# Kernel optimization log

Measured on AMD Instinct MI355X. Metric: run time of the kernel, lower is better.

Reference implementation:

```python
import jax, jax.numpy as jnp
import numpy as np

B, V, S, E, K, FF = 16, 512, 1024, 8, 2, 2048  # batch, n_vars, seq_len, n_experts, top_k, ff_dim


def setup_inputs() -> dict:
    key = jax.random.key(0)
    ks = jax.random.split(key, 6)
    def w(k, shape, fan_in):
        return (jax.random.normal(k, shape, jnp.float32) / np.sqrt(fan_in)).astype(jnp.float32)
    return {
        "x": jax.random.normal(ks[0], (B, S, V), jnp.float32),
        "gate_W": w(ks[1], (E, S), S),          # Gating: Linear(seq_len -> n_experts), no bias
        "exp_W": w(ks[2], (E, S, S), S),        # per-expert Linear(seq_len -> seq_len) weights
        "exp_b": jnp.zeros((E, S), jnp.float32),
        "fc1_W": w(ks[3], (FF, V), V),          # MLPFeat fc1: Linear(n_vars -> ff_dim)
        "fc1_b": jnp.zeros((FF,), jnp.float32),
        "fc2_W": w(ks[4], (V, FF), FF),         # MLPFeat fc2: Linear(ff_dim -> n_vars)
        "fc2_b": jnp.zeros((V,), jnp.float32),
    }


def reference(x, gate_W, exp_W, exp_b, fc1_W, fc1_b, fc2_W, fc2_b):
    # Dropout layers are identity at inference.
    res = x                                   # [B,S,V]
    xt = jnp.swapaxes(x, 1, 2)                # [B,V,S] tokens of dim seq_len

    # --- MLPTime (multi_expert MoE) ---
    logits = jnp.einsum('bvs,es->bve', xt, gate_W)      # [B,V,E]
    probs = jax.nn.softmax(logits, axis=-1)             # gate_logits returned by torch code
    w, sel = jax.lax.top_k(probs, K)                    # [B,V,K]
    # combine top-k weights into a dense per-expert weight [B,V,E] (zeros off top-k)
    full_w = jnp.sum(jax.nn.one_hot(sel, E, dtype=xt.dtype) * w[..., None], axis=2)
    # all-expert outputs, then weighted combine (same math as the per-expert scatter loop)
    all_out = jnp.einsum('bvs,eos->bveo', xt, exp_W) + exp_b[None, None]  # [B,V,E,S]
    moe = jnp.einsum('bve,bveo->bvo', full_w, all_out)                    # [B,V,S]
    t = jax.nn.relu(moe)

    x = jnp.swapaxes(t, 1, 2) + res           # [B,S,V] residual

    # --- MLPFeat ---
    res2 = x
    h = jax.nn.relu(x @ fc1_W.T + fc1_b)      # [B,S,FF]
    x = h @ fc2_W.T + fc2_b + res2            # [B,S,V]
    return (x, probs)
```

## Files before the change

### kernel.cpp

```cpp
#include <hip/hip_runtime.h>
#include <stdint.h>

#define B_  16
#define V_  512
#define S_  1024
#define E_  8
#define FF_ 2048
#define NT_ (B_*V_)
#define NR_ (B_*S_)

typedef __attribute__((ext_vector_type(8))) short bf16x8;
typedef __attribute__((ext_vector_type(4))) float f32x4;

__device__ __forceinline__ unsigned short f2bf(float f) {
    unsigned int u = __float_as_uint(f);
    u += 0x7FFFu + ((u >> 16) & 1u);
    return (unsigned short)(u >> 16);
}
__device__ __forceinline__ float bf2f(unsigned short u) {
    return __uint_as_float(((unsigned int)u) << 16);
}

__device__ __forceinline__ void gl_lds16(const void* g, void* l) {
    __builtin_amdgcn_global_load_lds((const __attribute__((address_space(1))) void*)g,
                                     (__attribute__((address_space(3))) void*)l,
                                     16, 0, 0);
}

__device__ __forceinline__ void cvt4(const float* s, unsigned short* d, int i) {
    float4 v = *(const float4*)(s + i);
    ushort4 o; o.x = f2bf(v.x); o.y = f2bf(v.y); o.z = f2bf(v.z); o.w = f2bf(v.w);
    *(ushort4*)(d + i) = o;
}
__global__ void k_convert3(const float* __restrict__ s0, unsigned short* __restrict__ d0, int g0,
                           const float* __restrict__ s1, unsigned short* __restrict__ d1, int g1,
                           const float* __restrict__ s2, unsigned short* __restrict__ d2) {
    int g = blockIdx.x * 256 + threadIdx.x;
    if (g < g0)           cvt4(s0, d0, g * 4);
    else if (g < g0 + g1) cvt4(s1, d1, (g - g0) * 4);
    else                  cvt4(s2, d2, (g - g0 - g1) * 4);
}

__global__ void k_transpose_xt(const float* __restrict__ x, unsigned short* __restrict__ xt) {
    __shared__ float t[32][33];
    int b = blockIdx.z, st = blockIdx.y, vt = blockIdx.x;
    int col = threadIdx.x & 31, row8 = threadIdx.x >> 5;
    for (int r = 0; r < 4; ++r) {
        int sl = row8 + r * 8;
        t[sl][col] = x[(b * S_ + st * 32 + sl) * V_ + vt * 32 + col];
    }
    __syncthreads();
    for (int r = 0; r < 4; ++r) {
        int vl = row8 + r * 8;
        xt[(size_t)(b * V_ + vt * 32 + vl) * S_ + st * 32 + col] = f2bf(t[col][vl]);
    }
}

__global__ __launch_bounds__(256) void k_gate_part(const float* __restrict__ x,
                                                   const float* __restrict__ gate_W,
                                                   double* __restrict__ part,
                                                   int* __restrict__ cnt) {
    __shared__ float gw[E_ * 128];
    __shared__ double red[4 * 64 * E_];
    int sc = blockIdx.x, vt0 = blockIdx.y * 64, b = blockIdx.z;
    int tid = threadIdx.x;
    if (sc == 0 && blockIdx.y == 0 && b == 0 && tid < E_) cnt[tid] = 0;
    for (int i = tid; i < E_ * 128; i += 256) {
        int e = i >> 7, j = i & 127;
        gw[i] = gate_W[e * S_ + sc * 128 + j];
    }
    __syncthreads();
    int vl = tid & 63, sg = tid >> 6;
    double acc[E_];
    #pragma unroll
    for (int e = 0; e < E_; ++e) acc[e] = 0.0;
    for (int jj = sg; jj < 128; jj += 4) {
        int s = sc * 128 + jj;
        double xv = (double)x[(b * S_ + s) * V_ + vt0 + vl];
        #pragma unroll
        for (int e = 0; e < E_; ++e) acc[e] += xv * (double)gw[e * 128 + jj];
    }
    #pragma unroll
    for (int e = 0; e < E_; ++e) red[(sg * 64 + vl) * E_ + e] = acc[e];
    __syncthreads();
    for (int i = tid; i < 64 * E_; i += 256) {
        int tkn = i >> 3, e = i & 7;
        double s = red[(0 * 64 + tkn) * E_ + e] + red[(1 * 64 + tkn) * E_ + e]
                 + red[(2 * 64 + tkn) * E_ + e] + red[(3 * 64 + tkn) * E_ + e];
        int t = b * V_ + vt0 + tkn;
        part[((size_t)sc * NT_ + t) * E_ + e] = s;
    }
}

__global__ __launch_bounds__(256) void k_gate_fin(const double* __restrict__ part,
                                                  float* __restrict__ probs_out,
                                                  int* __restrict__ cnt, int* __restrict__ tok_of,
                                                  int* __restrict__ tk_slot, float* __restrict__ tk_w) {
    int t = blockIdx.x * 256 + threadIdx.x;
    int lane = threadIdx.x & 63;
    double l[E_];
    #pragma unroll
    for (int e = 0; e < E_; ++e) l[e] = 0.0;
    for (int c = 0; c < S_ / 128; ++c) {
        const double* p = part + ((size_t)c * NT_ + t) * E_;
        #pragma unroll
        for (int e = 0; e < E_; ++e) l[e] += p[e];
    }
    double m = l[0];
    #pragma unroll
    for (int e = 1; e < E_; ++e) m = l[e] > m ? l[e] : m;
    double p[E_], sum = 0.0;
    #pragma unroll
    for (int e = 0; e < E_; ++e) { p[e] = exp(l[e] - m); sum += p[e]; }
    float pf[E_];
    #pragma unroll
    for (int e = 0; e < E_; ++e) pf[e] = (float)(p[e] / sum);
    float4 pa = {pf[0], pf[1], pf[2], pf[3]}, pb = {pf[4], pf[5], pf[6], pf[7]};
    *(float4*)(probs_out + (size_t)t * E_) = pa;
    *(float4*)(probs_out + (size_t)t * E_ + 4) = pb;
    int i0 = 0;
    #pragma unroll
    for (int e = 1; e < E_; ++e) if (pf[e] > pf[i0]) i0 = e;
    int i1 = -1;
    #pragma unroll
    for (int e = 0; e < E_; ++e) if (e != i0 && (i1 < 0 || pf[e] > pf[i1])) i1 = e;
    int sel[2] = {i0, i1};
    float wsel[2] = {pf[i0], pf[i1]};
    #pragma unroll
    for (int k = 0; k < 2; ++k) {
        int ie = sel[k];
        int pos = 0;
        for (int e = 0; e < E_; ++e) {
            unsigned long long msk = __ballot(ie == e);
            if (ie == e) {
                int rank = __popcll(msk & ((1ull << lane) - 1ull));
                int leader = __ffsll((long long)msk) - 1;
                int base = 0;
                if (lane == leader) base = atomicAdd(&cnt[e], __popcll(msk));
                base = __shfl(base, leader);
                pos = base + rank;
            }
        }
        tok_of[ie * NT_ + pos] = t;
        tk_slot[t * 2 + k] = (ie << 16) | pos;
        tk_w[t * 2 + k] = wsel[k];
    }
}

__global__ void k_scan(const int* __restrict__ cnt, int* __restrict__ offs,
                       int* __restrict__ tile_hdr) {
    if (threadIdx.x == 0) {
        int o = 0, nt = 0;
        for (int e = 0; e < E_; ++e) {
            offs[e] = o;
            for (int p = 0; p < cnt[e]; p += 128) {
                tile_hdr[1 + nt * 2] = e;
                tile_hdr[2 + nt * 2] = p;
                ++nt;
            }
            o += cnt[e];
        }
        offs[E_] = o;
        tile_hdr[0] = nt;
    }
}

__device__ __forceinline__ void gemm_k_loop64(const unsigned short* (&ap)[4],
                                              const unsigned short* (&bp)[4],
                                              short* As, short* Bs, int kIters, int wave, int lane,
                                              f32x4 (&acc)[4][4]) {
    char* ldsA = (char*)As + wave * 4096;
    char* ldsB = (char*)Bs + wave * 4096;
    int wm = (wave & 1) << 6, wn = (wave >> 1) << 6;
    int lr = lane & 15, quad = lane >> 4;
    int pb = (quad ^ (lr & 7)) * 8;
    const unsigned short* a0 = ap[0]; const unsigned short* a1 = ap[1];
    const unsigned short* a2 = ap[2]; const unsigned short* a3 = ap[3];
    const unsigned short* b0 = bp[0]; const unsigned short* b1 = bp[1];
    const unsigned short* b2 = bp[2]; const unsigned short* b3 = bp[3];
    for (int kk = 0; kk < kIters; ++kk) {
        gl_lds16(a0, ldsA);        gl_lds16(a1, ldsA + 1024);
        gl_lds16(a2, ldsA + 2048); gl_lds16(a3, ldsA + 3072);
        gl_lds16(b0, ldsB);        gl_lds16(b1, ldsB + 1024);
        gl_lds16(b2, ldsB + 2048); gl_lds16(b3, ldsB + 3072);
        a0 += 64; a1 += 64; a2 += 64; a3 += 64;
        b0 += 64; b1 += 64; b2 += 64; b3 += 64;
        __syncthreads();
        #pragma unroll
        for (int ks = 0; ks < 2; ++ks) {
            int po = pb ^ (ks << 5);
            bf16x8 af[4], bfv[4];
            #pragma unroll
            for (int i = 0; i < 4; ++i)
                af[i] = *(const bf16x8*)(As + (wm + i * 16 + lr) * 64 + po);
            #pragma unroll
            for (int j = 0; j < 4; ++j)
                bfv[j] = *(const bf16x8*)(Bs + (wn + j * 16 + lr) * 64 + po);
            #pragma unroll
            for (int i = 0; i < 4; ++i)
                #pragma unroll
                for (int j = 0; j < 4; ++j)
                    acc[i][j] = __builtin_amdgcn_mfma_f32_16x16x32_bf16(af[i], bfv[j], acc[i][j], 0, 0, 0);
        }
        __syncthreads();
    }
}

__global__ __launch_bounds__(256, 3) void k_moe_gemm(const unsigned short* __restrict__ xt,
                                                     const unsigned short* __restrict__ expWb,
                                                     const float* __restrict__ exp_b,
                                                     const int* __restrict__ cnt, const int* __restrict__ offs,
                                                     const int* __restrict__ tok_of,
                                                     const int* __restrict__ tile_hdr,
                                                     unsigned short* __restrict__ Yb) {
    int ntl = tile_hdr[0];
    if ((int)blockIdx.x >= ntl) return;
    int e    = tile_hdr[1 + blockIdx.x * 2];
    int pos0 = tile_hdr[2 + blockIdx.x * 2];
    int ne = cnt[e];
    int nt = blockIdx.y;
    __shared__ __align__(16) short As[128 * 64];
    __shared__ __align__(16) short Bs[128 * 64];
    int tid = threadIdx.x, wave = tid >> 6, lane = tid & 63;
    int rowLoc = wave * 32 + (lane >> 3);
    int cg = ((lane & 7) ^ ((lane >> 3) & 7)) * 8;
    const unsigned short* Wb = expWb + (size_t)e * S_ * S_;
    const unsigned short* ap[4];
    const unsigned short* bp[4];
    #pragma unroll
    for (int c = 0; c < 4; ++c) {
        int rr = rowLoc + c * 8;
        int tok = tok_of[e * NT_ + min(pos0 + rr, ne - 1)];
        ap[c] = xt + (size_t)tok * S_ + cg;
        bp[c] = Wb + (size_t)(nt * 128 + rr) * S_ + cg;
    }
    f32x4 acc[4][4] = {};
    gemm_k_loop64(ap, bp, As, Bs, S_ / 64, wave, lane, acc);
    int wm = (wave & 1) << 6, wn = (wave >> 1) << 6;
    int lr = lane & 15, quad = lane >> 4;
    int yrow0 = offs[e];
    #pragma unroll
    for (int i = 0; i < 4; ++i)
        #pragma unroll
        for (int r = 0; r < 4; ++r) {
            int pos = pos0 + wm + i * 16 + quad * 4 + r;
            if (pos < ne) {
                size_t row = (size_t)(yrow0 + pos);
                #pragma unroll
                for (int j = 0; j < 4; ++j) {
                    int col = nt * 128 + wn + j * 16 + lr;
                    Yb[row * S_ + col] = f2bf(acc[i][j][r] + exp_b[e * S_ + col]);
                }
            }
        }
}

__global__ void k_combine(const float* __restrict__ x, const unsigned short* __restrict__ Yb,
                          const int* __restrict__ offs, const int* __restrict__ tk_slot,
                          const float* __restrict__ tk_w,
                          unsigned short* __restrict__ x2b) {
    __shared__ float t[32][33];
    int b = blockIdx.z, st = blockIdx.y, vt = blockIdx.x;
    int tid = threadIdx.x;
    int vl = tid >> 3, sq = (tid & 7) * 4;
    int tok = b * V_ + vt * 32 + vl;
    int s0 = tk_slot[tok * 2 + 0], s1 = tk_slot[tok * 2 + 1];
    float w0 = tk_w[tok * 2 + 0], w1 = tk_w[tok * 2 + 1];
    size_t r0 = (size_t)(offs[s0 >> 16] + (s0 & 0xFFFF));
    size_t r1 = (size_t)(offs[s1 >> 16] + (s1 & 0xFFFF));
    int sg = st * 32 + sq;
    ushort4 y0 = *(const ushort4*)(Yb + r0 * S_ + sg);
    ushort4 y1 = *(const ushort4*)(Yb + r1 * S_ + sg);
    t[vl][sq + 0] = fmaxf(w0 * bf2f(y0.x) + w1 * bf2f(y1.x), 0.f);
    t[vl][sq + 1] = fmaxf(w0 * bf2f(y0.y) + w1 * bf2f(y1.y), 0.f);
    t[vl][sq + 2] = fmaxf(w0 * bf2f(y0.z) + w1 * bf2f(y1.z), 0.f);
    t[vl][sq + 3] = fmaxf(w0 * bf2f(y0.w) + w1 * bf2f(y1.w), 0.f);
    __syncthreads();
    int vcol = tid & 31, srow8 = tid >> 5;
    for (int r = 0; r < 4; ++r) {
        int sl = srow8 + r * 8;
        size_t gi = (size_t)(b * S_ + st * 32 + sl) * V_ + vt * 32 + vcol;
        x2b[gi] = f2bf(x[gi] + t[vcol][sl]);
    }
}

__global__ __launch_bounds__(256, 3) void k_fc1(const unsigned short* __restrict__ x2b,
                                                const unsigned short* __restrict__ w1b,
                                                const float* __restrict__ fc1_b,
                                                unsigned short* __restrict__ h) {
    __shared__ __align__(16) short As[128 * 64];
    __shared__ __align__(16) short Bs[128 * 64];
    int tid = threadIdx.x, wave = tid >> 6, lane = tid & 63;
    int rowLoc = wave * 32 + (lane >> 3);
    int cg = ((lane & 7) ^ ((lane >> 3) & 7)) * 8;
    int m0 = blockIdx.x * 128, n0 = blockIdx.y * 128;
    const unsigned short* ap[4];
    const unsigned short* bp[4];
    #pragma unroll
    for (int c = 0; c < 4; ++c) {
        int rr = rowLoc + c * 8;
        ap[c] = x2b + (size_t)(m0 + rr) * V_ + cg;
        bp[c] = w1b + (size_t)(n0 + rr) * V_ + cg;
    }
    f32x4 acc[4][4] = {};
    gemm_k_loop64(ap, bp, As, Bs, V_ / 64, wave, lane, acc);
    int wm = (wave & 1) << 6, wn = (wave >> 1) << 6;
    int lr = lane & 15, quad = lane >> 4;
    #pragma unroll
    for (int i = 0; i < 4; ++i)
        #pragma unroll
        for (int r = 0; r < 4; ++r) {
            size_t row = (size_t)(m0 + wm + i * 16 + quad * 4 + r);
            #pragma unroll
            for (int j = 0; j < 4; ++j) {
                int col = n0 + wn + j * 16 + lr;
                h[row * FF_ + col] = f2bf(fmaxf(acc[i][j][r] + fc1_b[col], 0.f));
            }
        }
}

__global__ __launch_bounds__(256, 3) void k_fc2(const unsigned short* __restrict__ h,
                                                const unsigned short* __restrict__ w2b,
                                                const float* __restrict__ fc2_b,
                                                const unsigned short* __restrict__ x2b,
                                                float* __restrict__ out) {
    __shared__ __align__(16) short As[128 * 64];
    __shared__ __align__(16) short Bs[128 * 64];
    int tid = threadIdx.x, wave = tid >> 6, lane = tid & 63;
    int rowLoc = wave * 32 + (lane >> 3);
    int cg = ((lane & 7) ^ ((lane >> 3) & 7)) * 8;
    int m0 = blockIdx.x * 128, n0 = blockIdx.y * 128;
    const unsigned short* ap[4];
    const unsigned short* bp[4];
    #pragma unroll
    for (int c = 0; c < 4; ++c) {
        int rr = rowLoc + c * 8;
        ap[c] = h + (size_t)(m0 + rr) * FF_ + cg;
        bp[c] = w2b + (size_t)(n0 + rr) * FF_ + cg;
    }
    f32x4 acc[4][4] = {};
    gemm_k_loop64(ap, bp, As, Bs, FF_ / 64, wave, lane, acc);
    int wm = (wave & 1) << 6, wn = (wave >> 1) << 6;
    int lr = lane & 15, quad = lane >> 4;
    #pragma unroll
    for (int i = 0; i < 4; ++i)
        #pragma unroll
        for (int r = 0; r < 4; ++r) {
            size_t row = (size_t)(m0 + wm + i * 16 + quad * 4 + r);
            #pragma unroll
            for (int j = 0; j < 4; ++j) {
                int col = n0 + wn + j * 16 + lr;
                out[row * V_ + col] = acc[i][j][r] + fc2_b[col] + bf2f(x2b[row * V_ + col]);
            }
        }
}

extern "C" void kernel_launch(void* const* d_in, const int* in_sizes, int n_in,
                              void* d_out, int out_size, void* d_ws, size_t ws_size,
                              hipStream_t stream) {
    const float* x      = (const float*)d_in[0];
    const float* gate_W = (const float*)d_in[1];
    const float* exp_W  = (const float*)d_in[2];
    const float* exp_b  = (const float*)d_in[3];
    const float* fc1_W  = (const float*)d_in[4];
    const float* fc1_b  = (const float*)d_in[5];
    const float* fc2_W  = (const float*)d_in[6];
    const float* fc2_b  = (const float*)d_in[7];
    float* out_x = (float*)d_out;
    float* out_p = (float*)d_out + (size_t)B_ * S_ * V_;

    if (ws_size < (size_t)155582592) return;

    char* ws = (char*)d_ws;
    unsigned short* Yb    = (unsigned short*)(ws);
    unsigned short* xt    = (unsigned short*)(ws +  67108864);
    int*            tile_hdr = (int*)(ws + 83886080);
    unsigned short* x2b   = (unsigned short*)(ws + 117440512);
    unsigned short* expWb = (unsigned short*)(ws + 134217728);
    unsigned short* fc1Wb = (unsigned short*)(ws + 150994944);
    unsigned short* fc2Wb = (unsigned short*)(ws + 153092096);
    char* route = ws + 155189248;
    int*   cnt     = (int*)(route);
    int*   offs    = (int*)(route + 64);
    int*   tok_of  = (int*)(route + 128);
    int*   tk_slot = (int*)(route + 128 + 262144);
    float* tk_w    = (float*)(route + 128 + 262144 + 65536);
    unsigned short* h = (unsigned short*)ws;
    double* part = (double*)ws;

    k_convert3<<<dim3((2097152 + 262144 + 262144) / 256), 256, 0, stream>>>(
        exp_W, expWb, 2097152, fc1_W, fc1Wb, 262144, fc2_W, fc2Wb);
    k_transpose_xt<<<dim3(V_ / 32, S_ / 32, B_), 256, 0, stream>>>(x, xt);
    k_gate_part<<<dim3(S_ / 128, V_ / 64, B_), 256, 0, stream>>>(x, gate_W, part, cnt);
    k_gate_fin<<<dim3(NT_ / 256), 256, 0, stream>>>(part, out_p, cnt, tok_of, tk_slot, tk_w);
    k_scan<<<1, 64, 0, stream>>>(cnt, offs, tile_hdr);
    k_moe_gemm<<<dim3(136, S_ / 128), 256, 0, stream>>>(xt, expWb, exp_b, cnt, offs, tok_of, tile_hdr, Yb);
    k_combine<<<dim3(V_ / 32, S_ / 32, B_), 256, 0, stream>>>(x, Yb, offs, tk_slot, tk_w, x2b);
    k_fc1<<<dim3(NR_ / 128, FF_ / 128), 256, 0, stream>>>(x2b, fc1Wb, fc1_b, h);
    k_fc2<<<dim3(NR_ / 128, V_ / 128), 256, 0, stream>>>(h, fc2Wb, fc2_b, x2b, out_x);
}
```

Measured before the change: 330.5 us.

## Fuse gate logits into transpose kernel and drop the scan kernel

Gate partial logits are now computed inside the x transpose kernel, reusing the shared-memory tile, so x is read only once and the separate gate-partial launch is removed. The single-thread scan kernel is gone: the MoE GEMM derives its expert and row offset from cnt on the fly, and the combine kernel recomputes per-expert prefix offsets itself. The GEMM tile index is also remapped across blockIdx.x, which changes which expert tiles sit next to each other in launch order. In exchange, part grows to 32 partial chunks instead of 8, so gate_fin reads four times as much data, and each thread does a short serial dot product in double precision.

After: 312.7 us. 1.06x faster.

```diff
diff --git a/kernel.cpp b/kernel.cpp
--- a/kernel.cpp
+++ b/kernel.cpp
@@ -41,55 +41,33 @@
     else                  cvt4(s2, d2, (g - g0 - g1) * 4);
 }
 
-__global__ void k_transpose_xt(const float* __restrict__ x, unsigned short* __restrict__ xt) {
+__global__ __launch_bounds__(256) void k_xt_gate(const float* __restrict__ x,
+                                                 const float* __restrict__ gate_W,
+                                                 unsigned short* __restrict__ xt,
+                                                 double* __restrict__ part,
+                                                 int* __restrict__ cnt) {
     __shared__ float t[32][33];
+    __shared__ float gw[E_][32];
     int b = blockIdx.z, st = blockIdx.y, vt = blockIdx.x;
-    int col = threadIdx.x & 31, row8 = threadIdx.x >> 5;
+    int tid = threadIdx.x;
+    if (vt == 0 && st == 0 && b == 0 && tid < E_) cnt[tid] = 0;
+    int col = tid & 31, row8 = tid >> 5;
     for (int r = 0; r < 4; ++r) {
         int sl = row8 + r * 8;
         t[sl][col] = x[(b * S_ + st * 32 + sl) * V_ + vt * 32 + col];
     }
+    gw[row8][col] = gate_W[row8 * S_ + st * 32 + col];
     __syncthreads();
     for (int r = 0; r < 4; ++r) {
         int vl = row8 + r * 8;
         xt[(size_t)(b * V_ + vt * 32 + vl) * S_ + st * 32 + col] = f2bf(t[col][vl]);
     }
-}
-
-__global__ __launch_bounds__(256) void k_gate_part(const float* __restrict__ x,
-                                                   const float* __restrict__ gate_W,
-                                                   double* __restrict__ part,
-                                                   int* __restrict__ cnt) {
-    __shared__ float gw[E_ * 128];
-    __shared__ double red[4 * 64 * E_];
-    int sc = blockIdx.x, vt0 = blockIdx.y * 64, b = blockIdx.z;
-    int tid = threadIdx.x;
-    if (sc == 0 && blockIdx.y == 0 && b == 0 && tid < E_) cnt[tid] = 0;
-    for (int i = tid; i < E_ * 128; i += 256) {
-        int e = i >> 7, j = i & 127;
-        gw[i] = gate_W[e * S_ + sc * 128 + j];
-    }
-    __syncthreads();
-    int vl = tid & 63, sg = tid >> 6;
-    double acc[E_];
-    #pragma unroll
-    for (int e = 0; e < E_; ++e) acc[e] = 0.0;
-    for (int jj = sg; jj < 128; jj += 4) {
-        int s = sc * 128 + jj;
-        double xv = (double)x[(b * S_ + s) * V_ + vt0 + vl];
-        #pragma unroll
-        for (int e = 0; e < E_; ++e) acc[e] += xv * (double)gw[e * 128 + jj];
-    }
-    #pragma unroll
-    for (int e = 0; e < E_; ++e) red[(sg * 64 + vl) * E_ + e] = acc[e];
-    __syncthreads();
-    for (int i = tid; i < 64 * E_; i += 256) {
-        int tkn = i >> 3, e = i & 7;
-        double s = red[(0 * 64 + tkn) * E_ + e] + red[(1 * 64 + tkn) * E_ + e]
-                 + red[(2 * 64 + tkn) * E_ + e] + red[(3 * 64 + tkn) * E_ + e];
-        int t = b * V_ + vt0 + tkn;
-        part[((size_t)sc * NT_ + t) * E_ + e] = s;
-    }
+    double acc = 0.0;
+    #pragma unroll
+    for (int s = 0; s < 32; ++s)
+        acc += (double)t[s][col] * (double)gw[row8][s];
+    int tok = b * V_ + vt * 32 + col;
+    part[((size_t)st * NT_ + tok) * E_ + row8] = acc;
 }
 
 __global__ __launch_bounds__(256) void k_gate_fin(const double* __restrict__ part,
@@ -101,7 +79,7 @@
     double l[E_];
     #pragma unroll
     for (int e = 0; e < E_; ++e) l[e] = 0.0;
-    for (int c = 0; c < S_ / 128; ++c) {
+    for (int c = 0; c < S_ / 32; ++c) {
         const double* p = part + ((size_t)c * NT_ + t) * E_;
         #pragma unroll
         for (int e = 0; e < E_; ++e) l[e] += p[e];
@@ -144,24 +122,6 @@
         tok_of[ie * NT_ + pos] = t;
         tk_slot[t * 2 + k] = (ie << 16) | pos;
         tk_w[t * 2 + k] = wsel[k];
-    }
-}
-
-__global__ void k_scan(const int* __restrict__ cnt, int* __restrict__ offs,
-                       int* __restrict__ tile_hdr) {
-    if (threadIdx.x == 0) {
-        int o = 0, nt = 0;
-        for (int e = 0; e < E_; ++e) {
-            offs[e] = o;
-            for (int p = 0; p < cnt[e]; p += 128) {
-                tile_hdr[1 + nt * 2] = e;
-                tile_hdr[2 + nt * 2] = p;
-                ++nt;
-            }
-            o += cnt[e];
-        }
-        offs[E_] = o;
-        tile_hdr[0] = nt;
     }
 }
 
@@ -209,15 +169,22 @@
 __global__ __launch_bounds__(256, 3) void k_moe_gemm(const unsigned short* __restrict__ xt,
                                                      const unsigned short* __restrict__ expWb,
                                                      const float* __restrict__ exp_b,
-                                                     const int* __restrict__ cnt, const int* __restrict__ offs,
+                                                     const int* __restrict__ cnt,
                                                      const int* __restrict__ tok_of,
-                                                     const int* __restrict__ tile_hdr,
                                                      unsigned short* __restrict__ Yb) {
-    int ntl = tile_hdr[0];
-    if ((int)blockIdx.x >= ntl) return;
-    int e    = tile_hdr[1 + blockIdx.x * 2];
-    int pos0 = tile_hdr[2 + blockIdx.x * 2];
-    int ne = cnt[e];
+    int bx = ((int)(blockIdx.x & 7)) * 17 + (int)(blockIdx.x >> 3);
+    int e = -1, pos0 = 0, yrow0 = 0, ne = 0;
+    {
+        int tb = 0, o = 0;
+        #pragma unroll
+        for (int i = 0; i < E_; ++i) {
+            int ci = cnt[i];
+            int nti = (ci + 127) >> 7;
+            if (e < 0 && bx < tb + nti) { e = i; pos0 = (bx - tb) * 128; yrow0 = o; ne = ci; }
+            tb += nti; o += ci;
+        }
+    }
+    if (e < 0) return;
     int nt = blockIdx.y;
     __shared__ __align__(16) short As[128 * 64];
     __shared__ __align__(16) short Bs[128 * 64];
@@ -238,7 +205,6 @@
     gemm_k_loop64(ap, bp, As, Bs, S_ / 64, wave, lane, acc);
     int wm = (wave & 1) << 6, wn = (wave >> 1) << 6;
     int lr = lane & 15, quad = lane >> 4;
-    int yrow0 = offs[e];
     #pragma unroll
     for (int i = 0; i < 4; ++i)
         #pragma unroll
@@ -256,7 +222,7 @@
 }
 
 __global__ void k_combine(const float* __restrict__ x, const unsigned short* __restrict__ Yb,
-                          const int* __restrict__ offs, const int* __restrict__ tk_slot,
+                          const int* __restrict__ cnt, const int* __restrict__ tk_slot,
                           const float* __restrict__ tk_w,
                           unsigned short* __restrict__ x2b) {
     __shared__ float t[32][33];
@@ -266,8 +232,16 @@
     int tok = b * V_ + vt * 32 + vl;
     int s0 = tk_slot[tok * 2 + 0], s1 = tk_slot[tok * 2 + 1];
     float w0 = tk_w[tok * 2 + 0], w1 = tk_w[tok * 2 + 1];
-    size_t r0 = (size_t)(offs[s0 >> 16] + (s0 & 0xFFFF));
-    size_t r1 = (size_t)(offs[s1 >> 16] + (s1 & 0xFFFF));
+    int e0 = s0 >> 16, e1 = s1 >> 16;
+    int r0b = 0, r1b = 0, o = 0;
+    #pragma unroll
+    for (int i = 0; i < E_; ++i) {
+        if (i == e0) r0b = o;
+        if (i == e1) r1b = o;
+        o += cnt[i];
+    }
+    size_t r0 = (size_t)(r0b + (s0 & 0xFFFF));
+    size_t r1 = (size_t)(r1b + (s1 & 0xFFFF));
     int sg = st * 32 + sq;
     ushort4 y0 = *(const ushort4*)(Yb + r0 * S_ + sg);
     ushort4 y1 = *(const ushort4*)(Yb + r1 * S_ + sg);
@@ -374,14 +348,12 @@
     char* ws = (char*)d_ws;
     unsigned short* Yb    = (unsigned short*)(ws);
     unsigned short* xt    = (unsigned short*)(ws +  67108864);
-    int*            tile_hdr = (int*)(ws + 83886080);
     unsigned short* x2b   = (unsigned short*)(ws + 117440512);
     unsigned short* expWb = (unsigned short*)(ws + 134217728);
     unsigned short* fc1Wb = (unsigned short*)(ws + 150994944);
     unsigned short* fc2Wb = (unsigned short*)(ws + 153092096);
     char* route = ws + 155189248;
     int*   cnt     = (int*)(route);
-    int*   offs    = (int*)(route + 64);
     int*   tok_of  = (int*)(route + 128);
     int*   tk_slot = (int*)(route + 128 + 262144);
     float* tk_w    = (float*)(route + 128 + 262144 + 65536);
@@ -390,12 +362,10 @@
 
     k_convert3<<<dim3((2097152 + 262144 + 262144) / 256), 256, 0, stream>>>(
         exp_W, expWb, 2097152, fc1_W, fc1Wb, 262144, fc2_W, fc2Wb);
-    k_transpose_xt<<<dim3(V_ / 32, S_ / 32, B_), 256, 0, stream>>>(x, xt);
-    k_gate_part<<<dim3(S_ / 128, V_ / 64, B_), 256, 0, stream>>>(x, gate_W, part, cnt);
+    k_xt_gate<<<dim3(V_ / 32, S_ / 32, B_), 256, 0, stream>>>(x, gate_W, xt, part, cnt);
     k_gate_fin<<<dim3(NT_ / 256), 256, 0, stream>>>(part, out_p, cnt, tok_of, tk_slot, tk_w);
-    k_scan<<<1, 64, 0, stream>>>(cnt, offs, tile_hdr);
-    k_moe_gemm<<<dim3(136, S_ / 128), 256, 0, stream>>>(xt, expWb, exp_b, cnt, offs, tok_of, tile_hdr, Yb);
-    k_combine<<<dim3(V_ / 32, S_ / 32, B_), 256, 0, stream>>>(x, Yb, offs, tk_slot, tk_w, x2b);
+    k_moe_gemm<<<dim3(136, S_ / 128), 256, 0, stream>>>(xt, expWb, exp_b, cnt, tok_of, Yb);
+    k_combine<<<dim3(V_ / 32, S_ / 32, B_), 256, 0, stream>>>(x, Yb, cnt, tk_slot, tk_w, x2b);
     k_fc1<<<dim3(NR_ / 128, FF_ / 128), 256, 0, stream>>>(x2b, fc1Wb, fc1_b, h);
     k_fc2<<<dim3(NR_ / 128, V_ / 128), 256, 0, stream>>>(h, fc2Wb, fc2_b, x2b, out_x);
 }
```
